# Kernel tuning notes

Measured on AMD Instinct MI355X. Metric: run time of the kernel, lower is better.

## Reference

```python
import jax, jax.numpy as jnp
import numpy as np

WIN = 4
HEAD_DIM = 32
N_HEADS = 6
TYPE = 'SW'
SHIFT = WIN // 2  # window_size // 2


def _relation():
    # [P, P, 3] relative coordinate indices into the (2w-1)^3 bias table
    cord = np.array([[i, j, k] for i in range(WIN) for j in range(WIN) for k in range(WIN)])
    return cord[:, None, :] - cord[None, :, :] + WIN - 1


def _shift_mask(nw):
    # boolean mask [nw^3, P, P]; True -> -inf (cross-boundary pairs in shifted windows)
    p, s = WIN, WIN - SHIFT
    m = np.zeros((nw, nw, nw, p, p, p, p, p, p), dtype=bool)
    m[-1, :, :, :s, :, :, s:, :, :] = True
    m[-1, :, :, s:, :, :, :s, :, :] = True
    m[:, -1, :, :, :s, :, :, s:, :] = True
    m[:, -1, :, :, s:, :, :, :s, :] = True
    m[:, :, -1, :, :, :s, :, :, s:] = True
    m[:, :, -1, :, :, s:, :, :, :s] = True
    return m.reshape(nw ** 3, p ** 3, p ** 3)


def setup_inputs() -> dict:
    key = jax.random.key(0)
    ks = jax.random.split(key, 6)
    dim = N_HEADS * HEAD_DIM  # 192
    B, S = 2, 32
    x = jax.random.normal(ks[0], (B, S, S, S, dim), jnp.float32)
    W_qkv = jax.random.normal(ks[1], (dim, 3 * dim), jnp.float32) * 0.02
    b_qkv = jnp.zeros((3 * dim,), jnp.float32)
    rel_params = jax.random.normal(ks[2], (N_HEADS, 2 * WIN - 1, 2 * WIN - 1, 2 * WIN - 1), jnp.float32) * 0.02
    W_out = jax.random.normal(ks[3], (dim, dim), jnp.float32) * 0.02
    b_out = jnp.zeros((dim,), jnp.float32)
    return {"x": x, "W_qkv": W_qkv, "b_qkv": b_qkv, "rel_params": rel_params, "W_out": W_out, "b_out": b_out}


def reference(x, W_qkv, b_qkv, rel_params, W_out, b_out):
    B, H, Wd, D, C = x.shape
    p = WIN
    nw = H // p
    scale = HEAD_DIM ** -0.5
    if TYPE != 'W':
        x = jnp.roll(x, (-SHIFT, -SHIFT, -SHIFT), axis=(1, 2, 3))
    # window partition: [B, NW, P, C], NW = nw^3, P = p^3
    xw = x.reshape(B, nw, p, nw, p, nw, p, C).transpose(0, 1, 3, 5, 2, 4, 6, 7).reshape(B, nw ** 3, p ** 3, C)
    qkv = xw @ W_qkv + b_qkv  # [B, NW, P, 3C]
    qkv = qkv.reshape(B, nw ** 3, p ** 3, 3 * N_HEADS, HEAD_DIM).transpose(3, 0, 1, 2, 4)  # [3h, B, NW, P, d]
    q, k, v = qkv[:N_HEADS], qkv[N_HEADS:2 * N_HEADS], qkv[2 * N_HEADS:]
    sim = jnp.einsum('hbwpc,hbwqc->hbwpq', q, k) * scale
    rel = _relation()
    bias = rel_params[:, rel[:, :, 0], rel[:, :, 1], rel[:, :, 2]]  # [h, P, P]
    sim = sim + bias[:, None, None, :, :]
    if TYPE != 'W':
        mask = jnp.asarray(_shift_mask(nw))[None, None]  # [1,1,NW,P,P]
        sim = jnp.where(mask, -jnp.inf, sim)
    probs = jax.nn.softmax(sim, axis=-1)
    out = jnp.einsum('hbwpq,hbwqc->hbwpc', probs, v)
    out = out.transpose(1, 2, 3, 0, 4).reshape(B, nw ** 3, p ** 3, C)  # h b w p c -> b w p (h c)
    out = out @ W_out + b_out
    out = out.reshape(B, nw, nw, nw, p, p, p, C).transpose(0, 1, 4, 2, 5, 3, 6, 7).reshape(B, H, Wd, D, C)
    if TYPE != 'W':
        out = jnp.roll(out, (SHIFT, SHIFT, SHIFT), axis=(1, 2, 3))
    return out
```

## Files before the change

kernel.cpp:

```cpp
#include <hip/hip_runtime.h>

typedef short bf16x8 __attribute__((ext_vector_type(8)));
typedef float f32x4 __attribute__((ext_vector_type(4)));
typedef unsigned short us4 __attribute__((ext_vector_type(4)));

#define MFMA16(a, b, c) __builtin_amdgcn_mfma_f32_16x16x32_bf16(a, b, c, 0, 0, 0)

__device__ __forceinline__ unsigned short f2bf(float f) {
    unsigned int u = __float_as_uint(f);
    u += 0x7FFFu + ((u >> 16) & 1u);
    return (unsigned short)(u >> 16);
}

#define WQT_OFF 0
#define WOT_OFF 221184
#define BQ_OFF  294912

__global__ void prep_kernel(const float* __restrict__ Wqkv,
                            const float* __restrict__ bqkv,
                            const float* __restrict__ Wout,
                            unsigned short* __restrict__ WqT,
                            unsigned short* __restrict__ WoT,
                            float* __restrict__ bq) {
    const float SCALE = 0.17677669529663687f;
    int i = blockIdx.x * 256 + threadIdx.x;
    if (i < 110592) {
        int n = i / 192, c = i - n * 192;
        float v = Wqkv[c * 576 + n];
        if (n < 192) v *= SCALE;
        WqT[i] = f2bf(v);
    } else if (i < 147456) {
        int j = i - 110592;
        int n = j / 192, c = j - n * 192;
        WoT[j] = f2bf(Wout[c * 192 + n]);
    } else if (i < 148032) {
        int n = i - 147456;
        float v = bqkv[n];
        if (n < 192) v *= SCALE;
        bq[n] = v;
    }
}

#define OFF_X   0
#define OFF_P   0
#define OFF_QK  13312
#define OFF_VT  38400
#define OFF_O   52224
#define OFF_RELF 65536
#define SMEM_US 69652

__global__ __launch_bounds__(512, 2) void wmsa_kernel(
    const float* __restrict__ x, const float* __restrict__ rel,
    const float* __restrict__ bout,
    const unsigned short* __restrict__ WqT,
    const unsigned short* __restrict__ WoT,
    const float* __restrict__ bq, float* __restrict__ out) {
    __shared__ __align__(16) unsigned short smem[SMEM_US];
    float* sRel = (float*)&smem[OFF_RELF];

    const int tid = threadIdx.x;
    const int bw = blockIdx.x;
    const int b  = bw >> 9;
    const int w  = bw & 511;
    const int wz = w >> 6, wy = (w >> 3) & 7, wx = w & 7;

    for (int i = tid; i < 2058; i += 512) sRel[i] = rel[i];
    {
        int t = tid >> 3, q8 = tid & 7;
        int tz = t >> 4, ty = (t >> 2) & 3, tx = t & 3;
        int gz = (wz * 4 + tz + 2) & 31;
        int gy = (wy * 4 + ty + 2) & 31;
        int gx = (wx * 4 + tx + 2) & 31;
        const float* xp = x + ((((b * 32 + gz) * 32 + gy) * 32 + gx)) * 192;
#pragma unroll
        for (int k = 0; k < 6; ++k) {
            int c = (q8 << 2) + (k << 5);
            float4 v = *(const float4*)(xp + c);
            us4 pk;
            pk[0] = f2bf(v.x); pk[1] = f2bf(v.y);
            pk[2] = f2bf(v.z); pk[3] = f2bf(v.w);
            *(us4*)&smem[OFF_X + t * 208 + c] = pk;
        }
    }
    __syncthreads();

    const int lane = tid & 63;
    const int wv   = tid >> 6;
    const int g    = lane >> 4;
    const int l15  = lane & 15;

    {
        bf16x8 afr[4][6];
#pragma unroll
        for (int m = 0; m < 4; ++m)
#pragma unroll
            for (int kk = 0; kk < 6; ++kk)
                afr[m][kk] = *(const bf16x8*)&smem[OFF_X + (m * 16 + l15) * 208 + kk * 32 + g * 8];

        int nb = wv;
        float bias = bq[nb * 16 + l15];
        bf16x8 bfr[6];
        {
            const unsigned short* wp = WqT + (nb * 16 + l15) * 192 + g * 8;
#pragma unroll
            for (int kk = 0; kk < 6; ++kk) bfr[kk] = *(const bf16x8*)(wp + kk * 32);
        }
        while (true) {
            int nbN = nb + 8;
            bool more = (nbN < 36);
            bf16x8 bfrN[6];
            float biasN = 0.f;
            if (more) {
                biasN = bq[nbN * 16 + l15];
                const unsigned short* wp = WqT + (nbN * 16 + l15) * 192 + g * 8;
#pragma unroll
                for (int kk = 0; kk < 6; ++kk) bfrN[kk] = *(const bf16x8*)(wp + kk * 32);
            }
            int colg = nb * 16 + l15;
            bool isV = (nb >= 24);
#pragma unroll
            for (int m = 0; m < 4; ++m) {
                f32x4 acc = {bias, bias, bias, bias};
#pragma unroll
                for (int kk = 0; kk < 6; ++kk) acc = MFMA16(afr[m][kk], bfr[kk], acc);
                int row0 = m * 16 + g * 4;
                if (!isV) {
#pragma unroll
                    for (int r = 0; r < 4; ++r)
                        smem[OFF_QK + (row0 + r) * 392 + colg] = f2bf(acc[r]);
                } else {
                    us4 pk;
#pragma unroll
                    for (int r = 0; r < 4; ++r) pk[r] = f2bf(acc[r]);
                    *(us4*)&smem[OFF_VT + (colg - 384) * 72 + row0] = pk;
                }
            }
            if (!more) break;
            nb = nbN;
            bias = biasN;
#pragma unroll
            for (int kk = 0; kk < 6; ++kk) bfr[kk] = bfrN[kk];
        }
    }
    __syncthreads();

    const bool sz = (wz == 7), sy = (wy == 7), sx = (wx == 7);
    {
        const int qy = (l15 >> 2) & 3, qx = l15 & 3;
        for (int it = wv * 3; it < wv * 3 + 3; ++it) {
            int h = it >> 2, mb = it & 3;
            bf16x8 qf = *(const bf16x8*)&smem[OFF_QK + (mb * 16 + l15) * 392 + h * 32 + g * 8];
            f32x4 s[4];
#pragma unroll
            for (int f = 0; f < 4; ++f) {
                bf16x8 kf = *(const bf16x8*)&smem[OFF_QK + (f * 16 + l15) * 392 + 192 + h * 32 + g * 8];
                f32x4 z = {0.f, 0.f, 0.f, 0.f};
                s[f] = MFMA16(qf, kf, z);
            }
#pragma unroll
            for (int f = 0; f < 4; ++f) {
                bool mz = sz && ((mb < 2) != (f < 2));
                bool my = sy && ((g < 2) != (qy < 2));
                int base = h * 343 + (mb - f + 3) * 49 + (g - qy + 3) * 7 + (3 - qx);
#pragma unroll
                for (int r = 0; r < 4; ++r) {
                    float v = s[f][r] + sRel[base + r];
                    bool mx = sx && ((r < 2) != (qx < 2));
                    s[f][r] = (mz | my | mx) ? -1e30f : v;
                }
            }
#pragma unroll
            for (int r = 0; r < 4; ++r) {
                float m0 = fmaxf(fmaxf(s[0][r], s[1][r]), fmaxf(s[2][r], s[3][r]));
#pragma unroll
                for (int d = 1; d < 16; d <<= 1) m0 = fmaxf(m0, __shfl_xor(m0, d, 64));
                float p0 = __expf(s[0][r] - m0);
                float p1 = __expf(s[1][r] - m0);
                float p2 = __expf(s[2][r] - m0);
                float p3 = __expf(s[3][r] - m0);
                float sm = p0 + p1 + p2 + p3;
#pragma unroll
                for (int d = 1; d < 16; d <<= 1) sm += __shfl_xor(sm, d, 64);
                float inv = 1.0f / sm;
                s[0][r] = p0 * inv; s[1][r] = p1 * inv;
                s[2][r] = p2 * inv; s[3][r] = p3 * inv;
            }
            unsigned short* pbase = &smem[OFF_P + wv * 1152];
#pragma unroll
            for (int f = 0; f < 4; ++f)
#pragma unroll
                for (int r = 0; r < 4; ++r)
                    pbase[(g * 4 + r) * 72 + f * 16 + l15] = f2bf(s[f][r]);
            f32x4 o0 = {0.f, 0.f, 0.f, 0.f}, o1 = {0.f, 0.f, 0.f, 0.f};
#pragma unroll
            for (int kt = 0; kt < 2; ++kt) {
                bf16x8 pf = *(const bf16x8*)&pbase[l15 * 72 + kt * 32 + g * 8];
                bf16x8 v0 = *(const bf16x8*)&smem[OFF_VT + (h * 32 + l15) * 72 + kt * 32 + g * 8];
                bf16x8 v1 = *(const bf16x8*)&smem[OFF_VT + (h * 32 + 16 + l15) * 72 + kt * 32 + g * 8];
                o0 = MFMA16(pf, v0, o0);
                o1 = MFMA16(pf, v1, o1);
            }
#pragma unroll
            for (int r = 0; r < 4; ++r) {
                smem[OFF_O + (mb * 16 + g * 4 + r) * 208 + h * 32 + l15]      = f2bf(o0[r]);
                smem[OFF_O + (mb * 16 + g * 4 + r) * 208 + h * 32 + 16 + l15] = f2bf(o1[r]);
            }
        }
    }
    __syncthreads();

    {
        int mw = wv >> 2, nq = wv & 3;
        bf16x8 ofr[2][6];
#pragma unroll
        for (int mi = 0; mi < 2; ++mi)
#pragma unroll
            for (int kk = 0; kk < 6; ++kk)
                ofr[mi][kk] = *(const bf16x8*)&smem[OFF_O + ((mw * 2 + mi) * 16 + l15) * 208 + kk * 32 + g * 8];
#pragma unroll
        for (int nbi = 0; nbi < 3; ++nbi) {
            int col = (nq + nbi * 4) * 16 + l15;
            float bo = bout[col];
            bf16x8 bfr[6];
            const unsigned short* wp = WoT + col * 192 + g * 8;
#pragma unroll
            for (int kk = 0; kk < 6; ++kk) bfr[kk] = *(const bf16x8*)(wp + kk * 32);
#pragma unroll
            for (int mi = 0; mi < 2; ++mi) {
                f32x4 acc = {bo, bo, bo, bo};
#pragma unroll
                for (int kk = 0; kk < 6; ++kk) acc = MFMA16(ofr[mi][kk], bfr[kk], acc);
                int m = mw * 2 + mi;
                int gz = (wz * 4 + m + 2) & 31;
                int gy = (wy * 4 + g + 2) & 31;
#pragma unroll
                for (int r = 0; r < 4; ++r) {
                    int gx = (wx * 4 + r + 2) & 31;
                    out[(((b * 32 + gz) * 32 + gy) * 32 + gx) * 192 + col] = acc[r];
                }
            }
        }
    }
}

extern "C" void kernel_launch(void* const* d_in, const int* in_sizes, int n_in,
                              void* d_out, int out_size, void* d_ws, size_t ws_size,
                              hipStream_t stream) {
    const float* x    = (const float*)d_in[0];
    const float* Wqkv = (const float*)d_in[1];
    const float* bqkv = (const float*)d_in[2];
    const float* rel  = (const float*)d_in[3];
    const float* Wout = (const float*)d_in[4];
    const float* bout = (const float*)d_in[5];

    unsigned short* WqT = (unsigned short*)((char*)d_ws + WQT_OFF);
    unsigned short* WoT = (unsigned short*)((char*)d_ws + WOT_OFF);
    float*          bq  = (float*)((char*)d_ws + BQ_OFF);
    float*          out = (float*)d_out;

    prep_kernel<<<579, 256, 0, stream>>>(Wqkv, bqkv, Wout, WqT, WoT, bq);
    wmsa_kernel<<<1024, 512, 0, stream>>>(x, rel, bout, WqT, WoT, bq, out);
}
```

Baseline: 176.8 us.

## Drop softmax max pass, use DPP sums, pack bf16 stores and prefetch weights

```diff
diff --git a/kernel.cpp b/kernel.cpp
--- a/kernel.cpp
+++ b/kernel.cpp
@@ -2,7 +2,6 @@
 
 typedef short bf16x8 __attribute__((ext_vector_type(8)));
 typedef float f32x4 __attribute__((ext_vector_type(4)));
-typedef unsigned short us4 __attribute__((ext_vector_type(4)));
 
 #define MFMA16(a, b, c) __builtin_amdgcn_mfma_f32_16x16x32_bf16(a, b, c, 0, 0, 0)
 
@@ -11,6 +10,18 @@
     u += 0x7FFFu + ((u >> 16) & 1u);
     return (unsigned short)(u >> 16);
 }
+__device__ __forceinline__ unsigned int f2bf2(float a, float b) {
+    unsigned int ua = __float_as_uint(a);
+    ua += 0x7FFFu + ((ua >> 16) & 1u);
+    unsigned int ub = __float_as_uint(b);
+    ub += 0x7FFFu + ((ub >> 16) & 1u);
+    return (ua >> 16) | (ub & 0xFFFF0000u);
+}
+#define DPPADD(v, CTRL)                                                        \
+    {                                                                          \
+        int _t = __builtin_amdgcn_mov_dpp(__float_as_int(v), CTRL, 0xf, 0xf, true); \
+        v += __int_as_float(_t);                                               \
+    }
 
 #define WQT_OFF 0
 #define WOT_OFF 221184
@@ -22,22 +33,39 @@
                             unsigned short* __restrict__ WqT,
                             unsigned short* __restrict__ WoT,
                             float* __restrict__ bq) {
-    const float SCALE = 0.17677669529663687f;
-    int i = blockIdx.x * 256 + threadIdx.x;
-    if (i < 110592) {
-        int n = i / 192, c = i - n * 192;
-        float v = Wqkv[c * 576 + n];
-        if (n < 192) v *= SCALE;
-        WqT[i] = f2bf(v);
-    } else if (i < 147456) {
-        int j = i - 110592;
-        int n = j / 192, c = j - n * 192;
-        WoT[j] = f2bf(Wout[c * 192 + n]);
-    } else if (i < 148032) {
-        int n = i - 147456;
-        float v = bqkv[n];
-        if (n < 192) v *= SCALE;
-        bq[n] = v;
+    __shared__ float tile[32][33];
+    const float SCALE = 0.17677669529663687f * 1.4426950408889634f;
+    int bid = blockIdx.x;
+    int tx = threadIdx.x & 31, ty = threadIdx.x >> 5;
+    if (bid < 108) {
+        int tn = bid % 18, tc = bid / 18;
+#pragma unroll
+        for (int i = 0; i < 4; ++i)
+            tile[ty + i * 8][tx] = Wqkv[(tc * 32 + ty + i * 8) * 576 + tn * 32 + tx];
+        __syncthreads();
+        bool isQ = (tn < 6);
+#pragma unroll
+        for (int i = 0; i < 4; ++i) {
+            float v = tile[tx][ty + i * 8];
+            if (isQ) v *= SCALE;
+            WqT[(tn * 32 + ty + i * 8) * 192 + tc * 32 + tx] = f2bf(v);
+        }
+    } else if (bid < 144) {
+        int bb = bid - 108;
+        int tn = bb % 6, tc = bb / 6;
+#pragma unroll
+        for (int i = 0; i < 4; ++i)
+            tile[ty + i * 8][tx] = Wout[(tc * 32 + ty + i * 8) * 192 + tn * 32 + tx];
+        __syncthreads();
+#pragma unroll
+        for (int i = 0; i < 4; ++i)
+            WoT[(tn * 32 + ty + i * 8) * 192 + tc * 32 + tx] = f2bf(tile[tx][ty + i * 8]);
+    } else {
+        for (int i = threadIdx.x; i < 576; i += 256) {
+            float v = bqkv[i];
+            if (i < 192) v *= SCALE;
+            bq[i] = v;
+        }
     }
 }
 
@@ -49,7 +77,7 @@
 #define OFF_RELF 65536
 #define SMEM_US 69652
 
-__global__ __launch_bounds__(512, 2) void wmsa_kernel(
+__global__ __launch_bounds__(512) void wmsa_kernel(
     const float* __restrict__ x, const float* __restrict__ rel,
     const float* __restrict__ bout,
     const unsigned short* __restrict__ WqT,
@@ -64,7 +92,12 @@
     const int w  = bw & 511;
     const int wz = w >> 6, wy = (w >> 3) & 7, wx = w & 7;
 
-    for (int i = tid; i < 2058; i += 512) sRel[i] = rel[i];
+    const int lane = tid & 63;
+    const int wv   = tid >> 6;
+    const int g    = lane >> 4;
+    const int l15  = lane & 15;
+
+    for (int i = tid; i < 2058; i += 512) sRel[i] = rel[i] * 1.4426950408889634f;
     {
         int t = tid >> 3, q8 = tid & 7;
         int tz = t >> 4, ty = (t >> 2) & 3, tx = t & 3;
@@ -76,18 +109,22 @@
         for (int k = 0; k < 6; ++k) {
             int c = (q8 << 2) + (k << 5);
             float4 v = *(const float4*)(xp + c);
-            us4 pk;
-            pk[0] = f2bf(v.x); pk[1] = f2bf(v.y);
-            pk[2] = f2bf(v.z); pk[3] = f2bf(v.w);
-            *(us4*)&smem[OFF_X + t * 208 + c] = pk;
-        }
+            uint2 pk;
+            pk.x = f2bf2(v.x, v.y);
+            pk.y = f2bf2(v.z, v.w);
+            *(uint2*)&smem[OFF_X + t * 208 + c] = pk;
+        }
+    }
+
+    int nb = wv;
+    float bias = bq[nb * 16 + l15];
+    bf16x8 bfr[6];
+    {
+        const unsigned short* wp = WqT + (nb * 16 + l15) * 192 + g * 8;
+#pragma unroll
+        for (int kk = 0; kk < 6; ++kk) bfr[kk] = *(const bf16x8*)(wp + kk * 32);
     }
     __syncthreads();
-
-    const int lane = tid & 63;
-    const int wv   = tid >> 6;
-    const int g    = lane >> 4;
-    const int l15  = lane & 15;
 
     {
         bf16x8 afr[4][6];
@@ -97,14 +134,6 @@
             for (int kk = 0; kk < 6; ++kk)
                 afr[m][kk] = *(const bf16x8*)&smem[OFF_X + (m * 16 + l15) * 208 + kk * 32 + g * 8];
 
-        int nb = wv;
-        float bias = bq[nb * 16 + l15];
-        bf16x8 bfr[6];
-        {
-            const unsigned short* wp = WqT + (nb * 16 + l15) * 192 + g * 8;
-#pragma unroll
-            for (int kk = 0; kk < 6; ++kk) bfr[kk] = *(const bf16x8*)(wp + kk * 32);
-        }
         while (true) {
             int nbN = nb + 8;
             bool more = (nbN < 36);
@@ -124,15 +153,17 @@
 #pragma unroll
                 for (int kk = 0; kk < 6; ++kk) acc = MFMA16(afr[m][kk], bfr[kk], acc);
                 int row0 = m * 16 + g * 4;
+                unsigned int u01 = f2bf2(acc[0], acc[1]);
+                unsigned int u23 = f2bf2(acc[2], acc[3]);
                 if (!isV) {
-#pragma unroll
-                    for (int r = 0; r < 4; ++r)
-                        smem[OFF_QK + (row0 + r) * 392 + colg] = f2bf(acc[r]);
+                    unsigned short* qk = &smem[OFF_QK + row0 * 392 + colg];
+                    qk[0]    = (unsigned short)u01;
+                    qk[392]  = (unsigned short)(u01 >> 16);
+                    qk[784]  = (unsigned short)u23;
+                    qk[1176] = (unsigned short)(u23 >> 16);
                 } else {
-                    us4 pk;
-#pragma unroll
-                    for (int r = 0; r < 4; ++r) pk[r] = f2bf(acc[r]);
-                    *(us4*)&smem[OFF_VT + (colg - 384) * 72 + row0] = pk;
+                    uint2 pk; pk.x = u01; pk.y = u23;
+                    *(uint2*)&smem[OFF_VT + (colg - 384) * 72 + row0] = pk;
                 }
             }
             if (!more) break;
@@ -147,6 +178,7 @@
     const bool sz = (wz == 7), sy = (wy == 7), sx = (wx == 7);
     {
         const int qy = (l15 >> 2) & 3, qx = l15 & 3;
+        unsigned short* pb = &smem[OFF_P + wv * 1152];
         for (int it = wv * 3; it < wv * 3 + 3; ++it) {
             int h = it >> 2, mb = it & 3;
             bf16x8 qf = *(const bf16x8*)&smem[OFF_QK + (mb * 16 + l15) * 392 + h * 32 + g * 8];
@@ -166,51 +198,67 @@
                 for (int r = 0; r < 4; ++r) {
                     float v = s[f][r] + sRel[base + r];
                     bool mx = sx && ((r < 2) != (qx < 2));
-                    s[f][r] = (mz | my | mx) ? -1e30f : v;
+                    v = (mz | my | mx) ? -1e30f : v;
+                    s[f][r] = exp2f(v);
                 }
             }
+            float inv[4];
 #pragma unroll
             for (int r = 0; r < 4; ++r) {
-                float m0 = fmaxf(fmaxf(s[0][r], s[1][r]), fmaxf(s[2][r], s[3][r]));
-#pragma unroll
-                for (int d = 1; d < 16; d <<= 1) m0 = fmaxf(m0, __shfl_xor(m0, d, 64));
-                float p0 = __expf(s[0][r] - m0);
-                float p1 = __expf(s[1][r] - m0);
-                float p2 = __expf(s[2][r] - m0);
-                float p3 = __expf(s[3][r] - m0);
-                float sm = p0 + p1 + p2 + p3;
-#pragma unroll
-                for (int d = 1; d < 16; d <<= 1) sm += __shfl_xor(sm, d, 64);
-                float inv = 1.0f / sm;
-                s[0][r] = p0 * inv; s[1][r] = p1 * inv;
-                s[2][r] = p2 * inv; s[3][r] = p3 * inv;
-            }
-            unsigned short* pbase = &smem[OFF_P + wv * 1152];
-#pragma unroll
-            for (int f = 0; f < 4; ++f)
-#pragma unroll
-                for (int r = 0; r < 4; ++r)
-                    pbase[(g * 4 + r) * 72 + f * 16 + l15] = f2bf(s[f][r]);
+                float sm = (s[0][r] + s[1][r]) + (s[2][r] + s[3][r]);
+                DPPADD(sm, 0xB1);
+                DPPADD(sm, 0x4E);
+                DPPADD(sm, 0x124);
+                DPPADD(sm, 0x128);
+                inv[r] = __builtin_amdgcn_rcpf(sm);
+            }
+#pragma unroll
+            for (int f = 0; f < 4; ++f) {
+                unsigned int u01 = f2bf2(s[f][0], s[f][1]);
+                unsigned int u23 = f2bf2(s[f][2], s[f][3]);
+                unsigned short* pw = &pb[(g * 4) * 72 + f * 16 + l15];
+                pw[0]   = (unsigned short)u01;
+                pw[72]  = (unsigned short)(u01 >> 16);
+                pw[144] = (unsigned short)u23;
+                pw[216] = (unsigned short)(u23 >> 16);
+            }
             f32x4 o0 = {0.f, 0.f, 0.f, 0.f}, o1 = {0.f, 0.f, 0.f, 0.f};
 #pragma unroll
             for (int kt = 0; kt < 2; ++kt) {
-                bf16x8 pf = *(const bf16x8*)&pbase[l15 * 72 + kt * 32 + g * 8];
+                bf16x8 pf = *(const bf16x8*)&pb[l15 * 72 + kt * 32 + g * 8];
                 bf16x8 v0 = *(const bf16x8*)&smem[OFF_VT + (h * 32 + l15) * 72 + kt * 32 + g * 8];
                 bf16x8 v1 = *(const bf16x8*)&smem[OFF_VT + (h * 32 + 16 + l15) * 72 + kt * 32 + g * 8];
                 o0 = MFMA16(pf, v0, o0);
                 o1 = MFMA16(pf, v1, o1);
             }
 #pragma unroll
-            for (int r = 0; r < 4; ++r) {
-                smem[OFF_O + (mb * 16 + g * 4 + r) * 208 + h * 32 + l15]      = f2bf(o0[r]);
-                smem[OFF_O + (mb * 16 + g * 4 + r) * 208 + h * 32 + 16 + l15] = f2bf(o1[r]);
-            }
-        }
+            for (int r = 0; r < 4; ++r) { o0[r] *= inv[r]; o1[r] *= inv[r]; }
+            unsigned int a0 = f2bf2(o0[0], o0[1]), a1 = f2bf2(o0[2], o0[3]);
+            unsigned int c0 = f2bf2(o1[0], o1[1]), c1 = f2bf2(o1[2], o1[3]);
+            unsigned short* ow = &smem[OFF_O + (mb * 16 + g * 4) * 208 + h * 32 + l15];
+            ow[0]        = (unsigned short)a0;
+            ow[208]      = (unsigned short)(a0 >> 16);
+            ow[416]      = (unsigned short)a1;
+            ow[624]      = (unsigned short)(a1 >> 16);
+            ow[16]       = (unsigned short)c0;
+            ow[16 + 208] = (unsigned short)(c0 >> 16);
+            ow[16 + 416] = (unsigned short)c1;
+            ow[16 + 624] = (unsigned short)(c1 >> 16);
+        }
+    }
+
+    const int mw = wv >> 2, nq = wv & 3;
+    int col0 = nq * 16 + l15;
+    float bo0 = bout[col0];
+    bf16x8 bfr0[6];
+    {
+        const unsigned short* wp = WoT + col0 * 192 + g * 8;
+#pragma unroll
+        for (int kk = 0; kk < 6; ++kk) bfr0[kk] = *(const bf16x8*)(wp + kk * 32);
     }
     __syncthreads();
 
     {
-        int mw = wv >> 2, nq = wv & 3;
         bf16x8 ofr[2][6];
 #pragma unroll
         for (int mi = 0; mi < 2; ++mi)
@@ -220,11 +268,18 @@
 #pragma unroll
         for (int nbi = 0; nbi < 3; ++nbi) {
             int col = (nq + nbi * 4) * 16 + l15;
-            float bo = bout[col];
+            float bo;
             bf16x8 bfr[6];
-            const unsigned short* wp = WoT + col * 192 + g * 8;
-#pragma unroll
-            for (int kk = 0; kk < 6; ++kk) bfr[kk] = *(const bf16x8*)(wp + kk * 32);
+            if (nbi == 0) {
+                bo = bo0;
+#pragma unroll
+                for (int kk = 0; kk < 6; ++kk) bfr[kk] = bfr0[kk];
+            } else {
+                bo = bout[col];
+                const unsigned short* wp = WoT + col * 192 + g * 8;
+#pragma unroll
+                for (int kk = 0; kk < 6; ++kk) bfr[kk] = *(const bf16x8*)(wp + kk * 32);
+            }
 #pragma unroll
             for (int mi = 0; mi < 2; ++mi) {
                 f32x4 acc = {bo, bo, bo, bo};
@@ -258,6 +313,6 @@
     float*          bq  = (float*)((char*)d_ws + BQ_OFF);
     float*          out = (float*)d_out;
 
-    prep_kernel<<<579, 256, 0, stream>>>(Wqkv, bqkv, Wout, WqT, WoT, bq);
+    prep_kernel<<<145, 256, 0, stream>>>(Wqkv, bqkv, Wout, WqT, WoT, bq);
     wmsa_kernel<<<1024, 512, 0, stream>>>(x, rel, bout, WqT, WoT, bq, out);
 }
```

Result: faster. 166.7 us (-5.7%).
